# Performance work log

Hardware: AMD Instinct MI355X
Metric: run time of the kernel (lower is better)

## Reference

```python
import jax, jax.numpy as jnp
import numpy as np

N_NODES = 8192
N_EDGES = 262144
D_IN = 512
D_OUT = 512


def setup_inputs() -> dict:
    key = jax.random.key(0)
    k1, k2, k3 = jax.random.split(key, 3)
    x = jax.random.normal(k1, (N_NODES, D_IN), dtype=jnp.float32)
    edge_index = jax.random.randint(k2, (2, N_EDGES), 0, N_NODES, dtype=jnp.int64)
    weight = jax.random.normal(k3, (D_IN, D_OUT), dtype=jnp.float32)
    bias = jnp.zeros((D_OUT,), dtype=jnp.float32)
    return {"x": x, "edge_index": edge_index, "weight": weight, "bias": bias}


def reference(x, edge_index, weight, bias):
    # GCN layer with selfloop=True branch of the original module.
    n = x.shape[0]
    # Dense symmetric adjacency via scatter-set, matching adj[ei0,ei1]=1; adj[ei1,ei0]=1
    adj = jnp.zeros((n, n), dtype=x.dtype)
    adj = adj.at[edge_index[0], edge_index[1]].set(1.0)
    adj = adj.at[edge_index[1], edge_index[0]].set(1.0)
    # Add self loops, symmetric degree normalization D^{-1/2} A D^{-1/2}
    adj = adj + jnp.eye(n, dtype=x.dtype)
    deg = jnp.sum(adj, axis=1)
    dinv = 1.0 / jnp.sqrt(deg)
    adj = adj * dinv[:, None] * dinv[None, :]  # == D @ adj @ D (diagonal scaling)
    return adj @ (x @ weight) + bias
```

## Files before the change

kernel.cpp:

```cpp
#include <hip/hip_runtime.h>
#include <hip/hip_bf16.h>


#define ELL_STRIDE 128

typedef __attribute__((ext_vector_type(8))) short bf16x8;
typedef __attribute__((ext_vector_type(4))) float f32x4;

__device__ __forceinline__ unsigned short f2bf(float f) {
  unsigned u = __float_as_uint(f);
  u = (u + 0x7fff + ((u >> 16) & 1)) >> 16;
  return (unsigned short)u;
}
__device__ __forceinline__ float bflo(unsigned u) {
  return __uint_as_float(u << 16);
}
__device__ __forceinline__ float bfhi(unsigned u) {
  return __uint_as_float(u & 0xffff0000u);
}

__global__ __launch_bounds__(256) void fused_front_kernel(
    const int* __restrict__ ei, unsigned* __restrict__ mask, int n_edges,
    int words,
    const float* __restrict__ x, unsigned short* __restrict__ xb, int n4,
    const float* __restrict__ W, unsigned short* __restrict__ Wt, int K, int N,
    unsigned short* __restrict__ Hs, float* __restrict__ dinv, int n_nodes,
    int edge_blocks, int cast_blocks, int tr_blocks) {
  const int bid = blockIdx.x;
  if (bid < edge_blocks) {
    const int e = bid * 256 + threadIdx.x;
    if (e < n_edges) {
      const int u = ei[e];
      const int v = ei[e + n_edges];
      atomicOr(&mask[(size_t)u * words + (v >> 5)], 1u << (v & 31));
      atomicOr(&mask[(size_t)v * words + (u >> 5)], 1u << (u & 31));
    }
    return;
  }
  if (bid < edge_blocks + cast_blocks) {
    const int t = (bid - edge_blocks) * 256 + threadIdx.x;
    if (t < n4) {
      float4 v = ((const float4*)x)[t];
      ushort4 o;
      o.x = f2bf(v.x); o.y = f2bf(v.y); o.z = f2bf(v.z); o.w = f2bf(v.w);
      ((ushort4*)xb)[t] = o;
    }
    return;
  }
  if (bid < edge_blocks + cast_blocks + tr_blocks) {
    __shared__ float tile[32][33];
    const int b = bid - edge_blocks - cast_blocks;
    const int bx = b & ((N >> 5) - 1);
    const int by = b >> (31 - __builtin_clz(N >> 5));
    const int tx = threadIdx.x & 31;
    const int ty = threadIdx.x >> 5;
#pragma unroll
    for (int r = 0; r < 4; ++r)
      tile[ty + 8 * r][tx] = W[(size_t)(by * 32 + ty + 8 * r) * N + bx * 32 + tx];
    __syncthreads();
#pragma unroll
    for (int r = 0; r < 4; ++r)
      Wt[(size_t)(bx * 32 + ty + 8 * r) * K + by * 32 + tx] =
          f2bf(tile[tx][ty + 8 * r]);
    return;
  }
  {
    const int t = threadIdx.x;
    if (t < (N >> 1)) ((unsigned*)(Hs + (size_t)n_nodes * N))[t] = 0;
    if (t == 0) dinv[n_nodes] = 0.f;
  }
}

__global__ __launch_bounds__(256) void fused_mid_kernel(
    const unsigned short* __restrict__ xb,
    const unsigned short* __restrict__ Wt,
    unsigned short* __restrict__ Hs,
    const unsigned* __restrict__ mask, unsigned short* __restrict__ ell,
    int* __restrict__ deg, float* __restrict__ dinv,
    int M, int N, int K, int words, int gemm_blocks, int nbx_sh) {
  __shared__ unsigned short As[512 * 8];
  __shared__ unsigned short Bs[512 * 8];

  const int tid = threadIdx.x;
  const int bid = blockIdx.x;

  if (bid < gemm_blocks) {
    const int wave = tid >> 6;
    const int lane = tid & 63;
    const int q = lane >> 4;
    const int c = lane & 15;
    const int bx = bid & ((1 << nbx_sh) - 1);
    const int by = bid >> nbx_sh;
    const int m0 = by * 64;
    const int n0 = bx * 64;
    const int wr = wave >> 1, wc = wave & 1;

    f32x4 acc[2][2] = {};

    for (int k0 = 0; k0 < K; k0 += 64) {
#pragma unroll
      for (int t = 0; t < 2; ++t) {
        const int sbase = t * 256 + wave * 64;
        const int s = sbase + lane;
        const unsigned short* g =
            xb + (size_t)(m0 + (s & 63)) * K + k0 + (s >> 6) * 8;
        __builtin_amdgcn_global_load_lds(
            (const __attribute__((address_space(1))) void*)g,
            (__attribute__((address_space(3))) void*)(As + sbase * 8), 16, 0, 0);
      }
#pragma unroll
      for (int t = 0; t < 2; ++t) {
        const int sbase = t * 256 + wave * 64;
        const int s = sbase + lane;
        const int bn = s >> 3;
        const int bk = (s & 7) ^ (bn & 7);
        const unsigned short* g =
            Wt + (size_t)(n0 + bn) * K + k0 + bk * 8;
        __builtin_amdgcn_global_load_lds(
            (const __attribute__((address_space(1))) void*)g,
            (__attribute__((address_space(3))) void*)(Bs + sbase * 8), 16, 0, 0);
      }
      __syncthreads();

#pragma unroll
      for (int kk = 0; kk < 2; ++kk) {
        bf16x8 a[2], b[2];
#pragma unroll
        for (int tm = 0; tm < 2; ++tm) {
          const int row = wr * 32 + tm * 16 + c;
          a[tm] = *(const bf16x8*)(As + (((kk * 4 + q) * 64) + row) * 8);
        }
#pragma unroll
        for (int tn = 0; tn < 2; ++tn) {
          const int n = wc * 32 + tn * 16 + c;
          b[tn] = *(const bf16x8*)(Bs + (n * 8 + ((kk * 4 + q) ^ (n & 7))) * 8);
        }
#pragma unroll
        for (int tm = 0; tm < 2; ++tm)
#pragma unroll
          for (int tn = 0; tn < 2; ++tn)
            acc[tm][tn] = __builtin_amdgcn_mfma_f32_16x16x32_bf16(
                a[tm], b[tn], acc[tm][tn], 0, 0, 0);
      }
      __syncthreads();
    }

#pragma unroll
    for (int tm = 0; tm < 2; ++tm) {
#pragma unroll
      for (int r = 0; r < 4; ++r) {
        const int grow = m0 + wr * 32 + tm * 16 + q * 4 + r;
#pragma unroll
        for (int tn = 0; tn < 2; ++tn) {
          const int gcol = n0 + wc * 32 + tn * 16 + c;
          Hs[(size_t)grow * N + gcol] = f2bf(acc[tm][tn][r]);
        }
      }
    }
    return;
  }

  {
    const int wave = tid >> 6, lane = tid & 63;
    const int node = (bid - gemm_blocks) * 4 + wave;
    const unsigned* __restrict__ row = mask + (size_t)node * words;
    unsigned short* __restrict__ out = ell + (size_t)node * ELL_STRIDE;

    int running = 0;
    for (int r = 0; r < words; r += 64) {
      const int w = r + lane;
      unsigned bits = row[w];
      const int cnt = __popc(bits);
      int x = cnt;
#pragma unroll
      for (int d = 1; d < 64; d <<= 1) {
        int y = __shfl_up(x, d, 64);
        if (lane >= d) x += y;
      }
      int pos = running + x - cnt;
      while (bits) {
        const int b = __builtin_ctz(bits);
        bits &= bits - 1;
        if (pos < ELL_STRIDE) out[pos] = (unsigned short)((w << 5) + b);
        ++pos;
      }
      running += __shfl(x, 63, 64);
    }
    for (int p = running + lane; p < ELL_STRIDE; p += 64)
      out[p] = (unsigned short)(p == running ? node : M);
    if (lane == 0) {
      const int dd = running + 1;
      deg[node] = dd < ELL_STRIDE ? dd : ELL_STRIDE;
      dinv[node] = rsqrtf((float)running + 1.0f);
    }
  }
}

__global__ __launch_bounds__(256) void spmm_kernel(
    const unsigned short* __restrict__ ell, const int* __restrict__ deg,
    const float* __restrict__ dinv, const unsigned short* __restrict__ Hs,
    const float* __restrict__ bias, float* __restrict__ out, int n, int D) {
  __shared__ uint2 ji[4][ELL_STRIDE];
  const int wave = threadIdx.x >> 6, lane = threadIdx.x & 63;
  const int bid = blockIdx.x;
  const int xcd = bid & 7;
  const int half = xcd >> 2;
  const int g = (bid >> 3) * 4 + (xcd & 3);
  const int i = g * 4 + wave;
  const unsigned rowbytes = (unsigned)(D * 2);

  {
    const unsigned j0 =
        __builtin_nontemporal_load(ell + (size_t)i * ELL_STRIDE + lane);
    const unsigned j1 =
        __builtin_nontemporal_load(ell + (size_t)i * ELL_STRIDE + 64 + lane);
    ji[wave][lane] = make_uint2(j0 * rowbytes, __float_as_uint(dinv[j0]));
    ji[wave][64 + lane] = make_uint2(j1 * rowbytes, __float_as_uint(dinv[j1]));
  }
  const int d = deg[i];
  const float di = dinv[i];
  const int kmax = (d + 7) & ~7;

  const char* __restrict__ hb = (const char*)Hs + half * D + lane * 8;
  float acc[4] = {0.f, 0.f, 0.f, 0.f};

#pragma unroll 8
  for (int k = 0; k < kmax; ++k) {
    const uint2 e = ji[wave][k];
    const float dj = __uint_as_float(e.y);
    const uint2 hv = *(const uint2*)(hb + e.x);
    acc[0] += dj * bflo(hv.x); acc[1] += dj * bfhi(hv.x);
    acc[2] += dj * bflo(hv.y); acc[3] += dj * bfhi(hv.y);
  }

  const int col = half * (D >> 1) + lane * 4;
  const float4 b0 = *(const float4*)(bias + col);
  f32x4 o0;
  o0.x = di * acc[0] + b0.x; o0.y = di * acc[1] + b0.y;
  o0.z = di * acc[2] + b0.z; o0.w = di * acc[3] + b0.w;
  __builtin_nontemporal_store(o0, (f32x4*)(out + (size_t)i * D + col));
}

extern "C" void kernel_launch(void* const* d_in, const int* in_sizes, int n_in,
                              void* d_out, int out_size, void* d_ws, size_t ws_size,
                              hipStream_t stream) {
  const float* x    = (const float*)d_in[0];
  const int*   ei   = (const int*)d_in[1];
  const float* W    = (const float*)d_in[2];
  const float* bias = (const float*)d_in[3];
  float* out = (float*)d_out;

  const int d_out_dim = in_sizes[3];
  const int d_in_dim  = in_sizes[2] / d_out_dim;
  const int n_nodes   = in_sizes[0] / d_in_dim;
  const int n_edges   = in_sizes[1] / 2;
  const int words     = (n_nodes + 31) / 32;

  char* ws = (char*)d_ws;
  size_t off = 0;
  unsigned* mask = (unsigned*)(ws + off); off += (size_t)n_nodes * words * 4;
  int* deg       = (int*)(ws + off);      off += (size_t)n_nodes * 4;
  float* dinv    = (float*)(ws + off);    off += (size_t)(n_nodes + 1) * 4;
  unsigned short* ell = (unsigned short*)(ws + off); off += (size_t)n_nodes * ELL_STRIDE * 2;
  unsigned short* xb  = (unsigned short*)(ws + off); off += (size_t)n_nodes * d_in_dim * 2;
  unsigned short* Wt  = (unsigned short*)(ws + off); off += (size_t)d_in_dim * d_out_dim * 2;
  unsigned short* Hs  = (unsigned short*)(ws + off);
  off += (size_t)(n_nodes + 1) * d_out_dim * 2;

  hipMemsetAsync(mask, 0, (size_t)n_nodes * words * 4, stream);

  const int edge_blocks = (n_edges + 255) / 256;
  const int n4 = n_nodes * d_in_dim / 4;
  const int cast_blocks = (n4 + 255) / 256;
  const int tr_blocks = (d_in_dim / 32) * (d_out_dim / 32);
  fused_front_kernel<<<edge_blocks + cast_blocks + tr_blocks + 1, 256, 0, stream>>>(
      ei, mask, n_edges, words, x, xb, n4, W, Wt, d_in_dim, d_out_dim,
      Hs, dinv, n_nodes, edge_blocks, cast_blocks, tr_blocks);

  const int nbx = d_out_dim / 64;
  const int nbx_sh = 31 - __builtin_clz(nbx);
  const int gemm_blocks = nbx * (n_nodes / 64);
  const int ell_blocks = n_nodes / 4;
  fused_mid_kernel<<<gemm_blocks + ell_blocks, 256, 0, stream>>>(
      xb, Wt, Hs, mask, ell, deg, dinv,
      n_nodes, d_out_dim, d_in_dim, words, gemm_blocks, nbx_sh);

  const int spmm_blocks = 2 * (n_nodes / 4);
  spmm_kernel<<<spmm_blocks, 256, 0, stream>>>(ell, deg, dinv, Hs, bias, out,
                                               n_nodes, d_out_dim);
}
```

Baseline: 161.4 us.

## Split SpMM rows into column quarters with four neighbors per wave iteration

The SpMM kernel now gives each wave a quarter of the output columns (128 bf16 = 256 bytes) instead of half. The 64 lanes form four 16-lane groups, and each group handles a different neighbor per iteration with 16-byte loads. Partial sums are combined across groups with xor shuffles, and the grid is doubled. The aim is wider loads and fewer serial loop iterations per row, which means more memory-level parallelism. The cost is the cross-lane reductions, each row's ELL slice being loaded four times, and only 16 lanes doing the stores.

```diff
diff --git a/kernel.cpp b/kernel.cpp
--- a/kernel.cpp
+++ b/kernel.cpp
@@ -204,9 +204,10 @@
   const int wave = threadIdx.x >> 6, lane = threadIdx.x & 63;
   const int bid = blockIdx.x;
   const int xcd = bid & 7;
-  const int half = xcd >> 2;
-  const int g = (bid >> 3) * 4 + (xcd & 3);
+  const int qt = xcd >> 1;
+  const int g = (bid >> 3) * 2 + (xcd & 1);
   const int i = g * 4 + wave;
+  const int e = lane >> 4, hl = lane & 15;
   const unsigned rowbytes = (unsigned)(D * 2);
 
   {
@@ -219,26 +220,40 @@
   }
   const int d = deg[i];
   const float di = dinv[i];
-  const int kmax = (d + 7) & ~7;
-
-  const char* __restrict__ hb = (const char*)Hs + half * D + lane * 8;
-  float acc[4] = {0.f, 0.f, 0.f, 0.f};
+  const int kmax = (d + 3) & ~3;
+
+  const char* __restrict__ hb = (const char*)Hs + qt * 256 + hl * 16;
+  float acc[8] = {0.f, 0.f, 0.f, 0.f, 0.f, 0.f, 0.f, 0.f};
 
 #pragma unroll 8
-  for (int k = 0; k < kmax; ++k) {
-    const uint2 e = ji[wave][k];
-    const float dj = __uint_as_float(e.y);
-    const uint2 hv = *(const uint2*)(hb + e.x);
+  for (int k = 0; k < kmax; k += 4) {
+    const uint2 t = ji[wave][k + e];
+    const float dj = __uint_as_float(t.y);
+    const uint4 hv = *(const uint4*)(hb + t.x);
     acc[0] += dj * bflo(hv.x); acc[1] += dj * bfhi(hv.x);
     acc[2] += dj * bflo(hv.y); acc[3] += dj * bfhi(hv.y);
-  }
-
-  const int col = half * (D >> 1) + lane * 4;
-  const float4 b0 = *(const float4*)(bias + col);
-  f32x4 o0;
-  o0.x = di * acc[0] + b0.x; o0.y = di * acc[1] + b0.y;
-  o0.z = di * acc[2] + b0.z; o0.w = di * acc[3] + b0.w;
-  __builtin_nontemporal_store(o0, (f32x4*)(out + (size_t)i * D + col));
+    acc[4] += dj * bflo(hv.z); acc[5] += dj * bfhi(hv.z);
+    acc[6] += dj * bflo(hv.w); acc[7] += dj * bfhi(hv.w);
+  }
+#pragma unroll
+  for (int t = 0; t < 8; ++t) {
+    acc[t] += __shfl_xor(acc[t], 16, 64);
+    acc[t] += __shfl_xor(acc[t], 32, 64);
+  }
+
+  if (lane < 16) {
+    const int col = qt * (D >> 2) + lane * 8;
+    const float4 b0 = *(const float4*)(bias + col);
+    const float4 b1 = *(const float4*)(bias + col + 4);
+    float* op = out + (size_t)i * D + col;
+    f32x4 o0, o1;
+    o0.x = di * acc[0] + b0.x; o0.y = di * acc[1] + b0.y;
+    o0.z = di * acc[2] + b0.z; o0.w = di * acc[3] + b0.w;
+    o1.x = di * acc[4] + b1.x; o1.y = di * acc[5] + b1.y;
+    o1.z = di * acc[6] + b1.z; o1.w = di * acc[7] + b1.w;
+    __builtin_nontemporal_store(o0, (f32x4*)op);
+    __builtin_nontemporal_store(o1, (f32x4*)(op + 4));
+  }
 }
 
 extern "C" void kernel_launch(void* const* d_in, const int* in_sizes, int n_in,
@@ -285,7 +300,7 @@
       xb, Wt, Hs, mask, ell, deg, dinv,
       n_nodes, d_out_dim, d_in_dim, words, gemm_blocks, nbx_sh);
 
-  const int spmm_blocks = 2 * (n_nodes / 4);
+  const int spmm_blocks = 4 * (n_nodes / 4);
   spmm_kernel<<<spmm_blocks, 256, 0, stream>>>(ell, deg, dinv, Hs, bias, out,
                                                n_nodes, d_out_dim);
 }
```

New measurement: 161.3 us. About the same (-0.0%).
